# Optimization experiments

Measured on AMD Instinct MI355X. Metric: run time of the kernel, lower is better.

Reference implementation:

```python
import jax, jax.numpy as jnp
import numpy as np

T_CONST = 0.1

def _hardtanh(w):
    # F.hardtanh(w, min_val=1e-10, max_val=1)
    return jnp.clip(w, 1e-10, 1.0)

def _forward(inp, hn, w_str2str, w_str2snr, w_m12m1, w_m12str, w_thal2m1,
             w_m12thal, w_thal2str, w_str2stn, w_stn2snr, w_snr2thal,
             str2str_fixed, inp_weight, mean_w, mean_b, std_w, std_b, hid_dim):
    H = hid_dim
    H5 = 5 * H
    Z = jnp.zeros((H, H), dtype=inp.dtype)
    n_inhib = int(0.3 * H)

    # Diagonal 'D' matrices realized as column scalings (D is diagonal)
    m12m1_d = jnp.concatenate([jnp.ones((H - n_inhib,)), -jnp.ones((n_inhib,))])

    # Block masks
    str2str_mask = jnp.zeros((H, H))
    m12str_mask = jnp.concatenate([jnp.ones((H, H - n_inhib)), jnp.zeros((H, n_inhib))], axis=1)
    str2stn_mask = jnp.concatenate([jnp.zeros((H, H // 2)), jnp.ones((H, H // 2))], axis=1)
    str2snr_mask = jnp.concatenate([jnp.ones((H, H // 2)), jnp.zeros((H, H // 2))], axis=1)

    # Region masks over the full 5H state
    thal_mask = jnp.concatenate([jnp.zeros((3 * H,)), jnp.ones((H,)), jnp.zeros((H,))])
    m1_mask = jnp.zeros((H5,))  # cat(zeros(4H), zeros(H)) in the source

    # Effective recurrent blocks (str2str_D = stn2snr_D = snr2thal_D = str2snr_D = -I)
    str2str_rec = -(str2str_mask * _hardtanh(w_str2str) + str2str_fixed)
    m12m1_rec = _hardtanh(w_m12m1) * m12m1_d[None, :]
    m12str_rec = m12str_mask * _hardtanh(w_m12str)
    str2snr_rec = -(str2snr_mask * _hardtanh(w_str2snr))
    thal2m1_rec = _hardtanh(w_thal2m1)
    m12thal_rec = _hardtanh(w_m12thal)
    thal2str_rec = _hardtanh(w_thal2str)
    str2stn_rec = str2stn_mask * _hardtanh(w_str2stn)
    stn2snr_rec = -_hardtanh(w_str2stn)  # NOTE: source uses str2stn weight here (faithful to original)
    snr2thal_rec = -_hardtanh(w_snr2thal)

    W_rec = jnp.concatenate([
        jnp.concatenate([str2str_rec, Z, Z, thal2str_rec, m12str_rec], axis=1),
        jnp.concatenate([str2stn_rec, Z, Z, Z, Z], axis=1),
        jnp.concatenate([str2snr_rec, stn2snr_rec, Z, Z, Z], axis=1),
        jnp.concatenate([Z, Z, snr2thal_rec, Z, m12thal_rec], axis=1),
        jnp.concatenate([Z, Z, Z, thal2m1_rec, m12m1_rec], axis=1),
    ], axis=0)  # [5H, 5H]

    # Precompute masked input drive for all timesteps: [T, B, 5H]
    u = jnp.einsum('bti,ih->tbh', inp, _hardtanh(inp_weight)) * thal_mask

    W_rec_T = W_rec.T

    def step(h, u_t):
        # (W_rec @ h.T).T == h @ W_rec.T
        h_new = jax.nn.relu((1.0 - T_CONST) * h + T_CONST * (h @ W_rec_T + u_t))
        return h_new, h_new

    _, hs = jax.lax.scan(step, hn[0], u)  # hs: [T, B, 5H]
    rnn_out = jnp.transpose(hs, (1, 0, 2))  # [B, T, 5H]
    hn_last = rnn_out[:, -1, :][None]  # [1, B, 5H]

    masked = rnn_out * m1_mask
    mean_out = masked @ mean_w + mean_b
    std_out = jnp.clip(masked @ std_w + std_b, -5.0, 10.0)
    return mean_out, std_out, rnn_out, hn_last


def setup_inputs() -> dict:
    H, B, T, I, A = 256, 64, 512, 4, 1
    H5 = 5 * H
    key = jax.random.key(0)
    ks = jax.random.split(key, 20)
    u01 = lambda k, shape, s: jax.random.uniform(k, shape, dtype=jnp.float32) * s
    inputs = {
        'inp': jax.random.uniform(ks[0], (B, T, I), dtype=jnp.float32),
        'hn': jnp.zeros((1, B, H5), dtype=jnp.float32),
        'w_str2str': u01(ks[1], (H, H), 0.01),
        'w_str2snr': u01(ks[2], (H, H), 0.01),
        'w_m12m1': u01(ks[3], (H, H), 0.01),
        'w_m12str': u01(ks[4], (H, H), 0.01),
        'w_thal2m1': u01(ks[5], (H, H), 0.01),
        'w_m12thal': u01(ks[6], (H, H), 0.01),
        'w_thal2str': u01(ks[7], (H, H), 0.01),
        'w_str2stn': u01(ks[8], (H, H), 0.01),
        'w_stn2snr': u01(ks[9], (H, H), 0.01),
        'w_snr2thal': u01(ks[10], (H, H), 0.01),
        'inp_weight': u01(ks[12], (I, H5), 0.1),
        'mean_w': jax.random.normal(ks[13], (H5, A), dtype=jnp.float32) * 0.02,
        'mean_b': jnp.zeros((A,), dtype=jnp.float32),
        'std_w': jax.random.normal(ks[14], (H5, A), dtype=jnp.float32) * 0.02,
        'std_b': jnp.zeros((A,), dtype=jnp.float32),
        'hid_dim': H,
    }
    keep = jax.random.bernoulli(ks[11], 0.15, (H, H)).astype(jnp.float32)
    inputs['str2str_fixed'] = u01(ks[15], (H, H), 0.01) * keep
    return inputs


def reference(inp, hn, w_str2str, w_str2snr, w_m12m1, w_m12str, w_thal2m1,
              w_m12thal, w_thal2str, w_str2stn, w_stn2snr, w_snr2thal,
              str2str_fixed, inp_weight, mean_w, mean_b, std_w, std_b, hid_dim):
    return _forward(inp, hn, w_str2str, w_str2snr, w_m12m1, w_m12str, w_thal2m1,
                    w_m12thal, w_thal2str, w_str2stn, w_stn2snr, w_snr2thal,
                    str2str_fixed, inp_weight, mean_w, mean_b, std_w, std_b, hid_dim)
```

## Files before the change

kernel.cpp:

```cpp
#include <hip/hip_runtime.h>

typedef unsigned short u16;
typedef __bf16 v8bf __attribute__((ext_vector_type(8)));
typedef float f32x4 __attribute__((ext_vector_type(4)));
typedef u16 u16x4 __attribute__((ext_vector_type(4)));

#define H5 1280
#define TT 512
#define NBLK 80
#define SPL 81920

#define OFF_W0 0
#define OFF_W1 3276800
#define OFF_W2 6553600
#define OFF_HS 9830400
#define OFF_WIN 10813440
#define OFF_CNT 10817536

#define MFMA(a, b, c) __builtin_amdgcn_mfma_f32_16x16x32_bf16(a, b, c, 0, 0, 0)

__device__ __forceinline__ float htanh_(float x) {
  return fminf(fmaxf(x, 1e-10f), 1.0f);
}
__device__ __forceinline__ u16 f2b(float f) {
  unsigned u = __float_as_uint(f);
  return (u16)((u + 0x7fffu + ((u >> 16) & 1u)) >> 16);
}
__device__ __forceinline__ float b2f(u16 b) {
  return __uint_as_float(((unsigned)b) << 16);
}

__global__ void build_w(const float* __restrict__ w_str2snr, const float* __restrict__ w_m12m1,
                        const float* __restrict__ w_m12str, const float* __restrict__ w_thal2m1,
                        const float* __restrict__ w_m12thal, const float* __restrict__ w_thal2str,
                        const float* __restrict__ w_str2stn, const float* __restrict__ w_snr2thal,
                        const float* __restrict__ fixedw, u16* __restrict__ W0,
                        u16* __restrict__ W1, u16* __restrict__ W2) {
  int idx = blockIdx.x * 256 + threadIdx.x;
  if (idx >= H5 * H5) return;
  int j = idx / H5, k = idx - j * H5;
  int jr = j >> 8, kr = k >> 8, kk = k & 255;
  int o = (j & 255) * 256 + kk;
  float w = 0.0f;
  if (jr == 0) {
    if (kr == 0) w = -fixedw[o];
    else if (kr == 3) w = htanh_(w_thal2str[o]);
    else if (kr == 4) w = (kk < 180) ? htanh_(w_m12str[o]) : 0.0f;
  } else if (jr == 1) {
    if (kr == 0) w = (kk >= 128) ? htanh_(w_str2stn[o]) : 0.0f;
  } else if (jr == 2) {
    if (kr == 0) w = (kk < 128) ? -htanh_(w_str2snr[o]) : 0.0f;
    else if (kr == 1) w = -htanh_(w_str2stn[o]);
  } else if (jr == 3) {
    if (kr == 2) w = -htanh_(w_snr2thal[o]);
    else if (kr == 4) w = htanh_(w_m12thal[o]);
  } else {
    if (kr == 3) w = htanh_(w_thal2m1[o]);
    else if (kr == 4) w = (kk < 180) ? htanh_(w_m12m1[o]) : -htanh_(w_m12m1[o]);
  }
  u16 c0 = f2b(w);  float r1 = w - b2f(c0);
  u16 c1 = f2b(r1); float r2 = r1 - b2f(c1);
  u16 c2 = f2b(r2);
  W0[idx] = c0; W1[idx] = c1; W2[idx] = c2;
}

__global__ void build_misc(const float* __restrict__ hn, const float* __restrict__ inp_weight,
                           const float* __restrict__ mean_b, const float* __restrict__ std_b,
                           float* __restrict__ out, u16* __restrict__ hs, float* __restrict__ Win) {
  int gid = blockIdx.x * 256 + threadIdx.x;
  if (gid < 65536) {
    out[gid] = (gid < 32768) ? mean_b[0] : fminf(10.0f, fmaxf(-5.0f, std_b[0]));
  } else if (gid < 65536 + SPL) {
    int i = gid - 65536;
    float v = hn[i];
    u16 c0 = f2b(v);  float r1 = v - b2f(c0);
    u16 c1 = f2b(r1); float r2 = r1 - b2f(c1);
    u16 c2 = f2b(r2);
    hs[i] = c0; hs[SPL + i] = c1; hs[2 * SPL + i] = c2;
  } else if (gid < 65536 + SPL + 1024) {
    int i = gid - 65536 - SPL;
    Win[i] = htanh_(inp_weight[(i >> 8) * H5 + 768 + (i & 255)]);
  }
}

__device__ __forceinline__ void tile_kb(int r, int (&kb)[3], int (&nch)[3]) {
  if (r == 0)      { kb[0] = 0;   nch[0] = 8; kb[1] = 768;  nch[1] = 8; kb[2] = 1024; nch[2] = 8; }
  else if (r == 1) { kb[0] = 128; nch[0] = 4; kb[1] = 0;    nch[1] = 0; kb[2] = 0;    nch[2] = 0; }
  else if (r == 2) { kb[0] = 0;   nch[0] = 4; kb[1] = 256;  nch[1] = 8; kb[2] = 0;    nch[2] = 0; }
  else if (r == 3) { kb[0] = 512; nch[0] = 8; kb[1] = 1024; nch[1] = 8; kb[2] = 0;    nch[2] = 0; }
  else             { kb[0] = 768; nch[0] = 8; kb[1] = 1024; nch[1] = 8; kb[2] = 0;    nch[2] = 0; }
}

__device__ __forceinline__ void load_afr(const u16* __restrict__ W0, const u16* __restrict__ W1,
                                         const u16* __restrict__ W2, int j0, int lr, int lk,
                                         const int (&kb)[3], const int (&nch)[3],
                                         v8bf (&afr)[3][8][3]) {
  const long jrow = (long)(j0 + lr) * H5 + lk;
#pragma unroll
  for (int q = 0; q < 3; ++q) {
    if (nch[q] > 0) {
#pragma unroll
      for (int c = 0; c < 8; ++c) {
        if (c < nch[q]) {
          long off = jrow + kb[q] + c * 32;
          afr[q][c][0] = *(const v8bf*)(W0 + off);
          afr[q][c][1] = *(const v8bf*)(W1 + off);
          afr[q][c][2] = *(const v8bf*)(W2 + off);
        }
      }
    }
  }
}

__device__ __forceinline__ f32x4 do_step(int t, int r, int b, int lk,
                                         const int (&kb)[3], const int (&nch)[3],
                                         const v8bf (&afr)[3][8][3], const float (&winreg)[4][4],
                                         const u16* __restrict__ hs_r,
                                         const float* __restrict__ inp_b, f32x4 hprev) {
  f32x4 a00 = {0.f, 0.f, 0.f, 0.f}, a01 = {0.f, 0.f, 0.f, 0.f};
  f32x4 a10 = {0.f, 0.f, 0.f, 0.f}, a11 = {0.f, 0.f, 0.f, 0.f};
#pragma unroll
  for (int q = 0; q < 3; ++q) {
    if (nch[q] > 0) {
      const u16* hb = hs_r + (long)b * H5 + kb[q] + lk;
#pragma unroll
      for (int c = 0; c < 8; ++c) {
        if (c < nch[q]) {
          v8bf h0 = *(const v8bf*)(hb + c * 32);
          v8bf h1 = *(const v8bf*)(hb + SPL + c * 32);
          v8bf h2 = *(const v8bf*)(hb + 2 * SPL + c * 32);
          if (c & 1) {
            a10 = MFMA(afr[q][c][0], h0, a10);
            a11 = MFMA(afr[q][c][0], h1, a11);
            a10 = MFMA(afr[q][c][1], h0, a10);
            a11 = MFMA(afr[q][c][1], h1, a11);
            a10 = MFMA(afr[q][c][2], h0, a10);
            a11 = MFMA(afr[q][c][0], h2, a11);
          } else {
            a00 = MFMA(afr[q][c][0], h0, a00);
            a01 = MFMA(afr[q][c][0], h1, a01);
            a00 = MFMA(afr[q][c][1], h0, a00);
            a01 = MFMA(afr[q][c][1], h1, a01);
            a00 = MFMA(afr[q][c][2], h0, a00);
            a01 = MFMA(afr[q][c][0], h2, a01);
          }
        }
      }
    }
  }
  f32x4 acc;
#pragma unroll
  for (int rr = 0; rr < 4; ++rr) acc[rr] = (a00[rr] + a01[rr]) + (a10[rr] + a11[rr]);
  if (r == 3) {
    const float* ip = inp_b + t * 4;
    float i0 = ip[0], i1 = ip[1], i2 = ip[2], i3 = ip[3];
#pragma unroll
    for (int rr = 0; rr < 4; ++rr)
      acc[rr] += i0 * winreg[0][rr] + i1 * winreg[1][rr] + i2 * winreg[2][rr] + i3 * winreg[3][rr];
  }
  f32x4 hnew;
#pragma unroll
  for (int rr = 0; rr < 4; ++rr)
    hnew[rr] = fmaxf(0.0f, 0.9f * hprev[rr] + 0.1f * acc[rr]);
  return hnew;
}

__device__ __forceinline__ void store_step(int t, int j0, int b, int hi, f32x4 hnew,
                                           float* __restrict__ rnn_b, u16* __restrict__ hs_w,
                                           float* __restrict__ hn_last) {
  *(f32x4*)(rnn_b + (long)t * H5 + j0 + hi * 4) = hnew;
  if (t < TT - 1) {
    u16x4 s0, s1, s2;
#pragma unroll
    for (int rr = 0; rr < 4; ++rr) {
      float v = hnew[rr];
      u16 c0 = f2b(v);  float r1 = v - b2f(c0);
      u16 c1 = f2b(r1); float r2 = r1 - b2f(c1);
      s0[rr] = c0; s1[rr] = c1; s2[rr] = f2b(r2);
    }
    u16* hw = hs_w + (long)b * H5 + j0 + hi * 4;
    *(u16x4*)(hw) = s0;
    *(u16x4*)(hw + SPL) = s1;
    *(u16x4*)(hw + 2 * SPL) = s2;
  } else {
    float* hl = hn_last + (long)b * H5 + j0 + hi * 4;
#pragma unroll
    for (int rr = 0; rr < 4; ++rr) hl[rr] = hnew[rr];
  }
}

__global__ void __launch_bounds__(256, 1)
rnn_pers(const float* __restrict__ inp, const float* __restrict__ hn,
         const u16* __restrict__ W0, const u16* __restrict__ W1, const u16* __restrict__ W2,
         u16* __restrict__ hs, float* __restrict__ rnn, float* __restrict__ hn_last,
         const float* __restrict__ Win, unsigned* __restrict__ counter) {
  const int lane = threadIdx.x & 63;
  const int lr = lane & 15, hi = lane >> 4, lk = hi * 8;
  const int jt = blockIdx.x;
  const int bt = threadIdx.x >> 6;
  const int r = jt >> 4;
  const int j0 = jt << 4;
  const int b = (bt << 4) + lr;

  int kb[3], nch[3];
  tile_kb(r, kb, nch);
  v8bf afr[3][8][3];
  load_afr(W0, W1, W2, j0, lr, lk, kb, nch, afr);

  float winreg[4][4];
  if (r == 3) {
#pragma unroll
    for (int i = 0; i < 4; ++i)
#pragma unroll
      for (int rr = 0; rr < 4; ++rr)
        winreg[i][rr] = Win[i * 256 + (j0 - 768) + hi * 4 + rr];
  }

  f32x4 hprev;
  {
    const float* hp = hn + (long)b * H5 + j0 + hi * 4;
#pragma unroll
    for (int rr = 0; rr < 4; ++rr) hprev[rr] = hp[rr];
  }

  float* rnn_b = rnn + (long)b * TT * H5;
  const float* inp_b = inp + (long)b * TT * 4;

  for (int t = 0; t < TT; ++t) {
    const u16* hs_r = hs + (t & 1) * (3 * SPL);
    u16* hs_w = hs + ((t & 1) ^ 1) * (3 * SPL);

    f32x4 hnew = do_step(t, r, b, lk, kb, nch, afr, winreg, hs_r, inp_b, hprev);
    store_step(t, j0, b, hi, hnew, rnn_b, hs_w, hn_last);
    hprev = hnew;

    if (t < TT - 1) {
      __syncthreads();
      if (threadIdx.x == 0) {
        __hip_atomic_fetch_add(counter, 1u, __ATOMIC_RELEASE, __HIP_MEMORY_SCOPE_AGENT);
        unsigned target = (unsigned)(t + 1) * NBLK;
        while (__hip_atomic_load(counter, __ATOMIC_RELAXED, __HIP_MEMORY_SCOPE_AGENT) < target)
          __builtin_amdgcn_s_sleep(2);
      }
      __syncthreads();
      __builtin_amdgcn_fence(__ATOMIC_ACQUIRE, "agent");
    }
  }
}

__global__ void __launch_bounds__(256, 1)
rnn_step(const float* __restrict__ inp, const float* __restrict__ hn,
         const u16* __restrict__ W0, const u16* __restrict__ W1, const u16* __restrict__ W2,
         u16* __restrict__ hs, float* __restrict__ rnn, float* __restrict__ hn_last,
         const float* __restrict__ Win, int t) {
  const int lane = threadIdx.x & 63;
  const int lr = lane & 15, hi = lane >> 4, lk = hi * 8;
  const int jt = blockIdx.x;
  const int bt = threadIdx.x >> 6;
  const int r = jt >> 4;
  const int j0 = jt << 4;
  const int b = (bt << 4) + lr;

  int kb[3], nch[3];
  tile_kb(r, kb, nch);
  v8bf afr[3][8][3];
  load_afr(W0, W1, W2, j0, lr, lk, kb, nch, afr);

  float winreg[4][4];
  if (r == 3) {
#pragma unroll
    for (int i = 0; i < 4; ++i)
#pragma unroll
      for (int rr = 0; rr < 4; ++rr)
        winreg[i][rr] = Win[i * 256 + (j0 - 768) + hi * 4 + rr];
  }

  f32x4 hprev;
  {
    const float* hp = (t == 0) ? (hn + (long)b * H5 + j0 + hi * 4)
                               : (rnn + ((long)b * TT + (t - 1)) * H5 + j0 + hi * 4);
#pragma unroll
    for (int rr = 0; rr < 4; ++rr) hprev[rr] = hp[rr];
  }

  const u16* hs_r = hs + (t & 1) * (3 * SPL);
  u16* hs_w = hs + ((t & 1) ^ 1) * (3 * SPL);
  float* rnn_b = rnn + (long)b * TT * H5;
  const float* inp_b = inp + (long)b * TT * 4;

  f32x4 hnew = do_step(t, r, b, lk, kb, nch, afr, winreg, hs_r, inp_b, hprev);
  store_step(t, j0, b, hi, hnew, rnn_b, hs_w, hn_last);
}

extern "C" void kernel_launch(void* const* d_in, const int* in_sizes, int n_in,
                              void* d_out, int out_size, void* d_ws, size_t ws_size,
                              hipStream_t stream) {
  const float* inp        = (const float*)d_in[0];
  const float* hn         = (const float*)d_in[1];
  const float* w_str2snr  = (const float*)d_in[3];
  const float* w_m12m1    = (const float*)d_in[4];
  const float* w_m12str   = (const float*)d_in[5];
  const float* w_thal2m1  = (const float*)d_in[6];
  const float* w_m12thal  = (const float*)d_in[7];
  const float* w_thal2str = (const float*)d_in[8];
  const float* w_str2stn  = (const float*)d_in[9];
  const float* w_snr2thal = (const float*)d_in[11];
  const float* inp_weight = (const float*)d_in[12];
  const float* mean_b     = (const float*)d_in[14];
  const float* std_b      = (const float*)d_in[16];
  const float* fixedw     = (const float*)d_in[18];

  char* ws = (char*)d_ws;
  u16* W0 = (u16*)(ws + OFF_W0);
  u16* W1 = (u16*)(ws + OFF_W1);
  u16* W2 = (u16*)(ws + OFF_W2);
  u16* hsb = (u16*)(ws + OFF_HS);
  float* Win = (float*)(ws + OFF_WIN);
  unsigned* cnt = (unsigned*)(ws + OFF_CNT);

  float* out = (float*)d_out;
  float* rnn = out + 65536;
  float* hnl = out + 65536 + 41943040;

  hipMemsetAsync(cnt, 0, 128, stream);
  build_w<<<6400, 256, 0, stream>>>(w_str2snr, w_m12m1, w_m12str, w_thal2m1, w_m12thal,
                                    w_thal2str, w_str2stn, w_snr2thal, fixedw, W0, W1, W2);
  build_misc<<<581, 256, 0, stream>>>(hn, inp_weight, mean_b, std_b, out, hsb, Win);

  void* args[] = {(void*)&inp, (void*)&hn, (void*)&W0, (void*)&W1, (void*)&W2, (void*)&hsb,
                  (void*)&rnn, (void*)&hnl, (void*)&Win, (void*)&cnt};
  hipError_t e = hipLaunchCooperativeKernel((const void*)rnn_pers, dim3(NBLK), dim3(256),
                                            args, 0, stream);
  if (e != hipSuccess) {
    for (int t = 0; t < TT; ++t)
      rnn_step<<<NBLK, 256, 0, stream>>>(inp, hn, W0, W1, W2, hsb, rnn, hnl, Win, t);
  }
}
```

Baseline: 8.860 ms.

## Specialize persistent RNN per region and replace acquire fence with coherent loads

```diff
diff --git a/kernel.cpp b/kernel.cpp
--- a/kernel.cpp
+++ b/kernel.cpp
@@ -1,6 +1,7 @@
 #include <hip/hip_runtime.h>
 
 typedef unsigned short u16;
+typedef unsigned long long u64;
 typedef __bf16 v8bf __attribute__((ext_vector_type(8)));
 typedef float f32x4 __attribute__((ext_vector_type(4)));
 typedef u16 u16x4 __attribute__((ext_vector_type(4)));
@@ -28,6 +29,18 @@
 }
 __device__ __forceinline__ float b2f(u16 b) {
   return __uint_as_float(((unsigned)b) << 16);
+}
+
+__device__ __forceinline__ v8bf ldh(const u16* p) {
+  union { u64 q[2]; v8bf v; } u;
+  u.q[0] = __hip_atomic_load((const u64*)p, __ATOMIC_RELAXED, __HIP_MEMORY_SCOPE_AGENT);
+  u.q[1] = __hip_atomic_load((const u64*)(p + 4), __ATOMIC_RELAXED, __HIP_MEMORY_SCOPE_AGENT);
+  return u.v;
+}
+__device__ __forceinline__ void sth(u16* p, u16x4 v) {
+  union { u16x4 s; u64 q; } u;
+  u.s = v;
+  __hip_atomic_store((u64*)p, u.q, __ATOMIC_RELAXED, __HIP_MEMORY_SCOPE_AGENT);
 }
 
 __global__ void build_w(const float* __restrict__ w_str2snr, const float* __restrict__ w_m12m1,
@@ -83,109 +96,160 @@
   }
 }
 
-__device__ __forceinline__ void tile_kb(int r, int (&kb)[3], int (&nch)[3]) {
-  if (r == 0)      { kb[0] = 0;   nch[0] = 8; kb[1] = 768;  nch[1] = 8; kb[2] = 1024; nch[2] = 8; }
-  else if (r == 1) { kb[0] = 128; nch[0] = 4; kb[1] = 0;    nch[1] = 0; kb[2] = 0;    nch[2] = 0; }
-  else if (r == 2) { kb[0] = 0;   nch[0] = 4; kb[1] = 256;  nch[1] = 8; kb[2] = 0;    nch[2] = 0; }
-  else if (r == 3) { kb[0] = 512; nch[0] = 8; kb[1] = 1024; nch[1] = 8; kb[2] = 0;    nch[2] = 0; }
-  else             { kb[0] = 768; nch[0] = 8; kb[1] = 1024; nch[1] = 8; kb[2] = 0;    nch[2] = 0; }
-}
-
-__device__ __forceinline__ void load_afr(const u16* __restrict__ W0, const u16* __restrict__ W1,
-                                         const u16* __restrict__ W2, int j0, int lr, int lk,
-                                         const int (&kb)[3], const int (&nch)[3],
-                                         v8bf (&afr)[3][8][3]) {
+template <int R> struct RC;
+template <> struct RC<0> { static constexpr int kb[3] = {0, 768, 1024}; static constexpr int nch[3] = {8, 8, 8}; };
+template <> struct RC<1> { static constexpr int kb[3] = {128, 0, 0};    static constexpr int nch[3] = {4, 0, 0}; };
+template <> struct RC<2> { static constexpr int kb[3] = {0, 256, 0};    static constexpr int nch[3] = {4, 8, 0}; };
+template <> struct RC<3> { static constexpr int kb[3] = {512, 1024, 0}; static constexpr int nch[3] = {8, 8, 0}; };
+template <> struct RC<4> { static constexpr int kb[3] = {768, 1024, 0}; static constexpr int nch[3] = {8, 8, 0}; };
+template <int R> constexpr int NCT = RC<R>::nch[0] + RC<R>::nch[1] + RC<R>::nch[2];
+
+template <int R>
+__device__ __forceinline__ void load_afr_t(const u16* __restrict__ W0, const u16* __restrict__ W1,
+                                           const u16* __restrict__ W2, int j0, int lr, int lk,
+                                           v8bf (&afr)[NCT<R>][3]) {
   const long jrow = (long)(j0 + lr) * H5 + lk;
+  int idx = 0;
 #pragma unroll
   for (int q = 0; q < 3; ++q) {
-    if (nch[q] > 0) {
-#pragma unroll
-      for (int c = 0; c < 8; ++c) {
-        if (c < nch[q]) {
-          long off = jrow + kb[q] + c * 32;
-          afr[q][c][0] = *(const v8bf*)(W0 + off);
-          afr[q][c][1] = *(const v8bf*)(W1 + off);
-          afr[q][c][2] = *(const v8bf*)(W2 + off);
+#pragma unroll
+    for (int c = 0; c < RC<R>::nch[q]; ++c) {
+      long off = jrow + RC<R>::kb[q] + c * 32;
+      afr[idx][0] = *(const v8bf*)(W0 + off);
+      afr[idx][1] = *(const v8bf*)(W1 + off);
+      afr[idx][2] = *(const v8bf*)(W2 + off);
+      ++idx;
+    }
+  }
+}
+
+template <int R>
+__device__ __forceinline__ f32x4 mfma_step_t(const u16* __restrict__ hs_r, int b, int lk,
+                                             const v8bf (&afr)[NCT<R>][3]) {
+  f32x4 a00 = {0.f, 0.f, 0.f, 0.f}, a01 = {0.f, 0.f, 0.f, 0.f};
+  f32x4 a10 = {0.f, 0.f, 0.f, 0.f}, a11 = {0.f, 0.f, 0.f, 0.f};
+  int idx = 0;
+#pragma unroll
+  for (int q = 0; q < 3; ++q) {
+    if (RC<R>::nch[q] > 0) {
+      const u16* hb = hs_r + (long)b * H5 + RC<R>::kb[q] + lk;
+#pragma unroll
+      for (int c = 0; c < RC<R>::nch[q]; ++c) {
+        v8bf h0 = ldh(hb + c * 32);
+        v8bf h1 = ldh(hb + SPL + c * 32);
+        v8bf h2 = ldh(hb + 2 * SPL + c * 32);
+        if (idx & 1) {
+          a10 = MFMA(afr[idx][0], h0, a10);
+          a11 = MFMA(afr[idx][0], h1, a11);
+          a10 = MFMA(afr[idx][1], h0, a10);
+          a11 = MFMA(afr[idx][1], h1, a11);
+          a10 = MFMA(afr[idx][2], h0, a10);
+          a11 = MFMA(afr[idx][0], h2, a11);
+        } else {
+          a00 = MFMA(afr[idx][0], h0, a00);
+          a01 = MFMA(afr[idx][0], h1, a01);
+          a00 = MFMA(afr[idx][1], h0, a00);
+          a01 = MFMA(afr[idx][1], h1, a01);
+          a00 = MFMA(afr[idx][2], h0, a00);
+          a01 = MFMA(afr[idx][0], h2, a01);
+        }
+        ++idx;
+      }
+    }
+  }
+  f32x4 acc;
+#pragma unroll
+  for (int rr = 0; rr < 4; ++rr) acc[rr] = (a00[rr] + a01[rr]) + (a10[rr] + a11[rr]);
+  return acc;
+}
+
+template <int R>
+__device__ void pers_loop(int j0, int b, int lr, int hi, int lk,
+                          const float* __restrict__ inp_b, const float* __restrict__ hn,
+                          const u16* __restrict__ W0, const u16* __restrict__ W1,
+                          const u16* __restrict__ W2, u16* __restrict__ hs,
+                          float* __restrict__ rnn_b, float* __restrict__ hn_last,
+                          const float* __restrict__ Win, unsigned* __restrict__ counter) {
+  v8bf afr[NCT<R>][3];
+  load_afr_t<R>(W0, W1, W2, j0, lr, lk, afr);
+
+  float winreg[4][4];
+  if constexpr (R == 3) {
+#pragma unroll
+    for (int i = 0; i < 4; ++i)
+#pragma unroll
+      for (int rr = 0; rr < 4; ++rr)
+        winreg[i][rr] = Win[i * 256 + (j0 - 768) + hi * 4 + rr];
+  }
+
+  f32x4 hprev;
+  {
+    const float* hp = hn + (long)b * H5 + j0 + hi * 4;
+#pragma unroll
+    for (int rr = 0; rr < 4; ++rr) hprev[rr] = hp[rr];
+  }
+
+  const u64 ca = (u64)counter;
+
+  for (int t = 0; t < TT; ++t) {
+    const u16* hs_r = hs + (t & 1) * (3 * SPL);
+    u16* hs_w = hs + ((t & 1) ^ 1) * (3 * SPL);
+
+    f32x4 acc = mfma_step_t<R>(hs_r, b, lk, afr);
+
+    if constexpr (R == 3) {
+      const float* ip = inp_b + t * 4;
+      float i0 = ip[0], i1 = ip[1], i2 = ip[2], i3 = ip[3];
+#pragma unroll
+      for (int rr = 0; rr < 4; ++rr)
+        acc[rr] += i0 * winreg[0][rr] + i1 * winreg[1][rr] + i2 * winreg[2][rr] + i3 * winreg[3][rr];
+    }
+
+    f32x4 hnew;
+#pragma unroll
+    for (int rr = 0; rr < 4; ++rr)
+      hnew[rr] = fmaxf(0.0f, 0.9f * hprev[rr] + 0.1f * acc[rr]);
+    hprev = hnew;
+
+    *(f32x4*)(rnn_b + (long)t * H5 + j0 + hi * 4) = hnew;
+
+    if (t < TT - 1) {
+      u16x4 s0, s1, s2;
+#pragma unroll
+      for (int rr = 0; rr < 4; ++rr) {
+        float v = hnew[rr];
+        u16 c0 = f2b(v);  float r1 = v - b2f(c0);
+        u16 c1 = f2b(r1); float r2 = r1 - b2f(c1);
+        s0[rr] = c0; s1[rr] = c1; s2[rr] = f2b(r2);
+      }
+      u16* hw = hs_w + (long)b * H5 + j0 + hi * 4;
+      sth(hw, s0);
+      sth(hw + SPL, s1);
+      sth(hw + 2 * SPL, s2);
+
+      asm volatile("s_waitcnt vmcnt(0)" ::: "memory");
+      __syncthreads();
+      if (threadIdx.x == 0) {
+        unsigned old;
+        asm volatile("global_atomic_add %0, %1, %2, off sc0 sc1\n\t"
+                     "s_waitcnt vmcnt(0)"
+                     : "=v"(old) : "v"(ca), "v"(1u) : "memory");
+        const unsigned target = (unsigned)(t + 1) * NBLK;
+        for (;;) {
+          unsigned cur;
+          asm volatile("global_load_dword %0, %1, off sc0 sc1\n\t"
+                       "s_waitcnt vmcnt(0)"
+                       : "=v"(cur) : "v"(ca) : "memory");
+          if (cur >= target) break;
+          __builtin_amdgcn_s_sleep(1);
         }
       }
+      __syncthreads();
+    } else {
+      float* hl = hn_last + (long)b * H5 + j0 + hi * 4;
+#pragma unroll
+      for (int rr = 0; rr < 4; ++rr) hl[rr] = hnew[rr];
     }
-  }
-}
-
-__device__ __forceinline__ f32x4 do_step(int t, int r, int b, int lk,
-                                         const int (&kb)[3], const int (&nch)[3],
-                                         const v8bf (&afr)[3][8][3], const float (&winreg)[4][4],
-                                         const u16* __restrict__ hs_r,
-                                         const float* __restrict__ inp_b, f32x4 hprev) {
-  f32x4 a00 = {0.f, 0.f, 0.f, 0.f}, a01 = {0.f, 0.f, 0.f, 0.f};
-  f32x4 a10 = {0.f, 0.f, 0.f, 0.f}, a11 = {0.f, 0.f, 0.f, 0.f};
-#pragma unroll
-  for (int q = 0; q < 3; ++q) {
-    if (nch[q] > 0) {
-      const u16* hb = hs_r + (long)b * H5 + kb[q] + lk;
-#pragma unroll
-      for (int c = 0; c < 8; ++c) {
-        if (c < nch[q]) {
-          v8bf h0 = *(const v8bf*)(hb + c * 32);
-          v8bf h1 = *(const v8bf*)(hb + SPL + c * 32);
-          v8bf h2 = *(const v8bf*)(hb + 2 * SPL + c * 32);
-          if (c & 1) {
-            a10 = MFMA(afr[q][c][0], h0, a10);
-            a11 = MFMA(afr[q][c][0], h1, a11);
-            a10 = MFMA(afr[q][c][1], h0, a10);
-            a11 = MFMA(afr[q][c][1], h1, a11);
-            a10 = MFMA(afr[q][c][2], h0, a10);
-            a11 = MFMA(afr[q][c][0], h2, a11);
-          } else {
-            a00 = MFMA(afr[q][c][0], h0, a00);
-            a01 = MFMA(afr[q][c][0], h1, a01);
-            a00 = MFMA(afr[q][c][1], h0, a00);
-            a01 = MFMA(afr[q][c][1], h1, a01);
-            a00 = MFMA(afr[q][c][2], h0, a00);
-            a01 = MFMA(afr[q][c][0], h2, a01);
-          }
-        }
-      }
-    }
-  }
-  f32x4 acc;
-#pragma unroll
-  for (int rr = 0; rr < 4; ++rr) acc[rr] = (a00[rr] + a01[rr]) + (a10[rr] + a11[rr]);
-  if (r == 3) {
-    const float* ip = inp_b + t * 4;
-    float i0 = ip[0], i1 = ip[1], i2 = ip[2], i3 = ip[3];
-#pragma unroll
-    for (int rr = 0; rr < 4; ++rr)
-      acc[rr] += i0 * winreg[0][rr] + i1 * winreg[1][rr] + i2 * winreg[2][rr] + i3 * winreg[3][rr];
-  }
-  f32x4 hnew;
-#pragma unroll
-  for (int rr = 0; rr < 4; ++rr)
-    hnew[rr] = fmaxf(0.0f, 0.9f * hprev[rr] + 0.1f * acc[rr]);
-  return hnew;
-}
-
-__device__ __forceinline__ void store_step(int t, int j0, int b, int hi, f32x4 hnew,
-                                           float* __restrict__ rnn_b, u16* __restrict__ hs_w,
-                                           float* __restrict__ hn_last) {
-  *(f32x4*)(rnn_b + (long)t * H5 + j0 + hi * 4) = hnew;
-  if (t < TT - 1) {
-    u16x4 s0, s1, s2;
-#pragma unroll
-    for (int rr = 0; rr < 4; ++rr) {
-      float v = hnew[rr];
-      u16 c0 = f2b(v);  float r1 = v - b2f(c0);
-      u16 c1 = f2b(r1); float r2 = r1 - b2f(c1);
-      s0[rr] = c0; s1[rr] = c1; s2[rr] = f2b(r2);
-    }
-    u16* hw = hs_w + (long)b * H5 + j0 + hi * 4;
-    *(u16x4*)(hw) = s0;
-    *(u16x4*)(hw + SPL) = s1;
-    *(u16x4*)(hw + 2 * SPL) = s2;
-  } else {
-    float* hl = hn_last + (long)b * H5 + j0 + hi * 4;
-#pragma unroll
-    for (int rr = 0; rr < 4; ++rr) hl[rr] = hnew[rr];
   }
 }
 
@@ -198,53 +262,77 @@
   const int lr = lane & 15, hi = lane >> 4, lk = hi * 8;
   const int jt = blockIdx.x;
   const int bt = threadIdx.x >> 6;
-  const int r = jt >> 4;
   const int j0 = jt << 4;
   const int b = (bt << 4) + lr;
-
-  int kb[3], nch[3];
-  tile_kb(r, kb, nch);
-  v8bf afr[3][8][3];
-  load_afr(W0, W1, W2, j0, lr, lk, kb, nch, afr);
-
+  float* rnn_b = rnn + (long)b * TT * H5;
+  const float* inp_b = inp + (long)b * TT * 4;
+  switch (jt >> 4) {
+    case 0: pers_loop<0>(j0, b, lr, hi, lk, inp_b, hn, W0, W1, W2, hs, rnn_b, hn_last, Win, counter); break;
+    case 1: pers_loop<1>(j0, b, lr, hi, lk, inp_b, hn, W0, W1, W2, hs, rnn_b, hn_last, Win, counter); break;
+    case 2: pers_loop<2>(j0, b, lr, hi, lk, inp_b, hn, W0, W1, W2, hs, rnn_b, hn_last, Win, counter); break;
+    case 3: pers_loop<3>(j0, b, lr, hi, lk, inp_b, hn, W0, W1, W2, hs, rnn_b, hn_last, Win, counter); break;
+    default: pers_loop<4>(j0, b, lr, hi, lk, inp_b, hn, W0, W1, W2, hs, rnn_b, hn_last, Win, counter); break;
+  }
+}
+
+template <int R>
+__device__ void step_one(int t, int j0, int b, int lr, int hi, int lk,
+                         const float* __restrict__ inp_b, const float* __restrict__ hn,
+                         const u16* __restrict__ W0, const u16* __restrict__ W1,
+                         const u16* __restrict__ W2, u16* __restrict__ hs,
+                         float* __restrict__ rnn, float* __restrict__ rnn_b,
+                         float* __restrict__ hn_last, const float* __restrict__ Win) {
+  v8bf afr[NCT<R>][3];
+  load_afr_t<R>(W0, W1, W2, j0, lr, lk, afr);
   float winreg[4][4];
-  if (r == 3) {
+  if constexpr (R == 3) {
 #pragma unroll
     for (int i = 0; i < 4; ++i)
 #pragma unroll
       for (int rr = 0; rr < 4; ++rr)
         winreg[i][rr] = Win[i * 256 + (j0 - 768) + hi * 4 + rr];
   }
-
   f32x4 hprev;
   {
-    const float* hp = hn + (long)b * H5 + j0 + hi * 4;
+    const float* hp = (t == 0) ? (hn + (long)b * H5 + j0 + hi * 4)
+                               : (rnn + ((long)b * TT + (t - 1)) * H5 + j0 + hi * 4);
 #pragma unroll
     for (int rr = 0; rr < 4; ++rr) hprev[rr] = hp[rr];
   }
-
-  float* rnn_b = rnn + (long)b * TT * H5;
-  const float* inp_b = inp + (long)b * TT * 4;
-
-  for (int t = 0; t < TT; ++t) {
-    const u16* hs_r = hs + (t & 1) * (3 * SPL);
-    u16* hs_w = hs + ((t & 1) ^ 1) * (3 * SPL);
-
-    f32x4 hnew = do_step(t, r, b, lk, kb, nch, afr, winreg, hs_r, inp_b, hprev);
-    store_step(t, j0, b, hi, hnew, rnn_b, hs_w, hn_last);
-    hprev = hnew;
-
-    if (t < TT - 1) {
-      __syncthreads();
-      if (threadIdx.x == 0) {
-        __hip_atomic_fetch_add(counter, 1u, __ATOMIC_RELEASE, __HIP_MEMORY_SCOPE_AGENT);
-        unsigned target = (unsigned)(t + 1) * NBLK;
-        while (__hip_atomic_load(counter, __ATOMIC_RELAXED, __HIP_MEMORY_SCOPE_AGENT) < target)
-          __builtin_amdgcn_s_sleep(2);
-      }
-      __syncthreads();
-      __builtin_amdgcn_fence(__ATOMIC_ACQUIRE, "agent");
+  const u16* hs_r = hs + (t & 1) * (3 * SPL);
+  u16* hs_w = hs + ((t & 1) ^ 1) * (3 * SPL);
+
+  f32x4 acc = mfma_step_t<R>(hs_r, b, lk, afr);
+  if constexpr (R == 3) {
+    const float* ip = inp_b + t * 4;
+    float i0 = ip[0], i1 = ip[1], i2 = ip[2], i3 = ip[3];
+#pragma unroll
+    for (int rr = 0; rr < 4; ++rr)
+      acc[rr] += i0 * winreg[0][rr] + i1 * winreg[1][rr] + i2 * winreg[2][rr] + i3 * winreg[3][rr];
+  }
+  f32x4 hnew;
+#pragma unroll
+  for (int rr = 0; rr < 4; ++rr)
+    hnew[rr] = fmaxf(0.0f, 0.9f * hprev[rr] + 0.1f * acc[rr]);
+
+  *(f32x4*)(rnn_b + (long)t * H5 + j0 + hi * 4) = hnew;
+  if (t < TT - 1) {
+    u16x4 s0, s1, s2;
+#pragma unroll
+    for (int rr = 0; rr < 4; ++rr) {
+      float v = hnew[rr];
+      u16 c0 = f2b(v);  float r1 = v - b2f(c0);
+      u16 c1 = f2b(r1); float r2 = r1 - b2f(c1);
+      s0[rr] = c0; s1[rr] = c1; s2[rr] = f2b(r2);
     }
+    u16* hw = hs_w + (long)b * H5 + j0 + hi * 4;
+    sth(hw, s0);
+    sth(hw + SPL, s1);
+    sth(hw + 2 * SPL, s2);
+  } else {
+    float* hl = hn_last + (long)b * H5 + j0 + hi * 4;
+#pragma unroll
+    for (int rr = 0; rr < 4; ++rr) hl[rr] = hnew[rr];
   }
 }
 
@@ -257,39 +345,17 @@
   const int lr = lane & 15, hi = lane >> 4, lk = hi * 8;
   const int jt = blockIdx.x;
   const int bt = threadIdx.x >> 6;
-  const int r = jt >> 4;
   const int j0 = jt << 4;
   const int b = (bt << 4) + lr;
-
-  int kb[3], nch[3];
-  tile_kb(r, kb, nch);
-  v8bf afr[3][8][3];
-  load_afr(W0, W1, W2, j0, lr, lk, kb, nch, afr);
-
-  float winreg[4][4];
-  if (r == 3) {
-#pragma unroll
-    for (int i = 0; i < 4; ++i)
-#pragma unroll
-      for (int rr = 0; rr < 4; ++rr)
-        winreg[i][rr] = Win[i * 256 + (j0 - 768) + hi * 4 + rr];
-  }
-
-  f32x4 hprev;
-  {
-    const float* hp = (t == 0) ? (hn + (long)b * H5 + j0 + hi * 4)
-                               : (rnn + ((long)b * TT + (t - 1)) * H5 + j0 + hi * 4);
-#pragma unroll
-    for (int rr = 0; rr < 4; ++rr) hprev[rr] = hp[rr];
-  }
-
-  const u16* hs_r = hs + (t & 1) * (3 * SPL);
-  u16* hs_w = hs + ((t & 1) ^ 1) * (3 * SPL);
   float* rnn_b = rnn + (long)b * TT * H5;
   const float* inp_b = inp + (long)b * TT * 4;
-
-  f32x4 hnew = do_step(t, r, b, lk, kb, nch, afr, winreg, hs_r, inp_b, hprev);
-  store_step(t, j0, b, hi, hnew, rnn_b, hs_w, hn_last);
+  switch (jt >> 4) {
+    case 0: step_one<0>(t, j0, b, lr, hi, lk, inp_b, hn, W0, W1, W2, hs, rnn, rnn_b, hn_last, Win); break;
+    case 1: step_one<1>(t, j0, b, lr, hi, lk, inp_b, hn, W0, W1, W2, hs, rnn, rnn_b, hn_last, Win); break;
+    case 2: step_one<2>(t, j0, b, lr, hi, lk, inp_b, hn, W0, W1, W2, hs, rnn, rnn_b, hn_last, Win); break;
+    case 3: step_one<3>(t, j0, b, lr, hi, lk, inp_b, hn, W0, W1, W2, hs, rnn, rnn_b, hn_last, Win); break;
+    default: step_one<4>(t, j0, b, lr, hi, lk, inp_b, hn, W0, W1, W2, hs, rnn, rnn_b, hn_last, Win); break;
+  }
 }
 
 extern "C" void kernel_launch(void* const* d_in, const int* in_sizes, int n_in,
```

After: 10.02 ms. 1.13x slower.
